# Kernel optimization log

Measured on AMD Instinct MI355X. Metric: run time of the kernel, lower is better.

Reference implementation:

```python
import jax, jax.numpy as jnp
import numpy as np

NUM_BINS = 8
TAIL = 3.0
MBW = 1e-3  # min_bin_width
MBH = 1e-3  # min_bin_height
MD = 1e-3   # min_derivative
B, C, H, W = 16, 12, 128, 128
COND = C // 3
HID = 64
STEP = 3 * NUM_BINS - 1
OUT = C * STEP


def setup_inputs() -> dict:
    key = jax.random.key(0)
    ks = jax.random.split(key, 8)
    s = lambda k, shape, scale=1.0: jax.random.normal(k, shape, jnp.float32) * scale
    return {
        'x': s(ks[0], (B, C, H, W)),
        'logdet': jnp.zeros((B,), jnp.float32),
        'conditioning': s(ks[1], (B, COND, H, W)),
        'W1': s(ks[2], (HID, C + COND, 3, 3), 0.05), 'b1': jnp.zeros((HID,), jnp.float32),
        'W2': s(ks[3], (HID, HID, 1, 1), 0.05), 'b2': jnp.zeros((HID,), jnp.float32),
        'W3': s(ks[4], (OUT, HID, 3, 3), 0.05), 'b3': jnp.zeros((OUT,), jnp.float32),
    }


def _conv(x, w, b, pad):
    y = jax.lax.conv_general_dilated(x, w, (1, 1), [(pad, pad), (pad, pad)],
                                     dimension_numbers=('NCHW', 'OIHW', 'NCHW'))
    return y + b[None, :, None, None]


def _checker_mask(h, w, parity):
    ii, jj = jnp.meshgrid(jnp.arange(h), jnp.arange(w), indexing='ij')
    m = jnp.where((ii + jj) % 2 == 0, parity, 1 - parity)
    return m.astype(jnp.float32)[None, None]  # (1,1,H,W)


def _rqs_forward(x, uw, uh, ud):
    # x: (B,C,H,W); uw/uh: (...,K); ud: (...,K-1). 'linear' tails, tail_bound=TAIL.
    K = NUM_BINS
    left, right = -TAIL, TAIL
    inside = (x >= left) & (x <= right)
    xc = jnp.clip(x, left, right)

    w = MBW + (1.0 - MBW * K) * jax.nn.softmax(uw, axis=-1)
    cw = jnp.pad(jnp.cumsum(w, -1), [(0, 0)] * (w.ndim - 1) + [(1, 0)])
    cw = (right - left) * cw + left
    cw = cw.at[..., 0].set(left).at[..., -1].set(right)
    w = cw[..., 1:] - cw[..., :-1]

    h = MBH + (1.0 - MBH * K) * jax.nn.softmax(uh, axis=-1)
    ch = jnp.pad(jnp.cumsum(h, -1), [(0, 0)] * (h.ndim - 1) + [(1, 0)])
    ch = (right - left) * ch + left
    ch = ch.at[..., 0].set(left).at[..., -1].set(right)
    h = ch[..., 1:] - ch[..., :-1]

    const = float(np.log(np.expm1(1.0 - MD)))  # boundary derivative -> 1 under linear tails
    udp = jnp.pad(ud, [(0, 0)] * (ud.ndim - 1) + [(1, 1)], constant_values=const)
    d = MD + jax.nn.softplus(udp)  # (...,K+1)

    delta = h / w
    # searchsorted: bin index per element
    idx = jnp.clip(jnp.sum((xc[..., None] >= cw).astype(jnp.int32), -1) - 1, 0, K - 1)[..., None]
    g = lambda t: jnp.take_along_axis(t, idx, axis=-1)[..., 0]

    icw, iw = g(cw), g(w)
    ich, ih = g(ch), g(h)
    idl = g(delta)
    id0 = g(d)
    id1 = g(d[..., 1:])

    theta = (xc - icw) / iw
    t1 = theta * (1.0 - theta)
    num = ih * (idl * theta ** 2 + id0 * t1)
    den = idl + (id0 + id1 - 2.0 * idl) * t1
    y = ich + num / den
    dnum = idl ** 2 * (id1 * theta ** 2 + 2.0 * idl * t1 + id0 * (1.0 - theta) ** 2)
    lad = jnp.log(dnum) - 2.0 * jnp.log(den)
    return jnp.where(inside, y, x), jnp.where(inside, lad, 0.0)


def reference(x, logdet, conditioning, W1, b1, W2, b2, W3, b3):
    mask = _checker_mask(H, W, 0)
    x_frozen = mask * x
    x_active = (1.0 - mask) * x
    z = jnp.concatenate([x_frozen, conditioning], axis=1)
    h1 = jax.nn.relu(_conv(z, W1, b1, 1))
    h2 = jax.nn.relu(_conv(h1, W2, b2, 0))
    params = _conv(h2, W3, b3, 1)  # (B, C*STEP, H, W)
    # all channels at once instead of python loop over C
    p = params.reshape(B, C, STEP, H, W).transpose(0, 1, 3, 4, 2)  # (B,C,H,W,STEP)
    uw = p[..., :NUM_BINS]
    uh = p[..., NUM_BINS:2 * NUM_BINS]
    ud = p[..., 2 * NUM_BINS:]
    y, lad = _rqs_forward(x_active, uw, uh, ud)
    x_out = x_frozen + y  # matches original: frozen part + spline output (no re-masking of y)
    logdet_out = logdet + lad.sum(axis=(1, 2, 3))
    return x_out, logdet_out
```

## Files before the change

### kernel.cpp

```cpp
#include <hip/hip_runtime.h>

#define HW (128*128)

typedef __bf16 bf16x8 __attribute__((ext_vector_type(8)));
typedef float  float4v __attribute__((ext_vector_type(4)));
typedef int    int4v   __attribute__((ext_vector_type(4)));
typedef int    int2v   __attribute__((ext_vector_type(2)));

static __device__ __forceinline__ short f2bf(float f) {
    unsigned u = __float_as_uint(f);
    unsigned r = (u + 0x7FFFu + ((u >> 16) & 1u)) >> 16;
    return (short)(r & 0xFFFFu);
}
static __device__ __forceinline__ int pack2(short a, short b) {
    return (int)((unsigned short)a | ((unsigned)(unsigned short)b << 16));
}
static __device__ __forceinline__ void async_cp16(const void* g, void* l) {
    __builtin_amdgcn_global_load_lds(
        (const __attribute__((address_space(1))) unsigned int*)g,
        (__attribute__((address_space(3))) unsigned int*)l, 16, 0, 0);
}

__global__ __launch_bounds__(256) void prep_weights(
    const float* __restrict__ W1, const float* __restrict__ W2,
    const float* __restrict__ W3,
    short* __restrict__ W1sw, short* __restrict__ W2sw, short* __restrict__ W3g,
    char* __restrict__ h2p, int4v* __restrict__ zerobuf)
{
    int tid = blockIdx.x * 256 + threadIdx.x;
    int stride = gridDim.x * 256;
    for (int i = tid; i < 5*256*8; i += stride) {
        int e = i & 7, q = (i >> 3) & 255, s = i >> 11;
        int n = q >> 2, c = q & 3;
        int gc = c ^ ((n >> 1) & 3);
        int tap = 2*s + (gc >> 1);
        int ch = (gc & 1)*8 + e;
        float v = 0.f;
        if (tap < 9) {
            int ky = (tap*11) >> 5; int kx = tap - 3*ky;
            v = W1[((n*16 + ch)*3 + ky)*3 + kx];
        }
        W1sw[i] = f2bf(v);
    }
    for (int i = tid; i < 2*256*8; i += stride) {
        int e = i & 7, q = (i >> 3) & 255, s = i >> 11;
        int n = q >> 2, c = q & 3;
        int gc = c ^ ((n >> 1) & 3);
        int k = s*32 + gc*8 + e;
        W2sw[i] = f2bf(W2[n*64 + k]);
    }
    for (int i = tid; i < 165888; i += stride) {
        int e = i & 7;
        int n = (i >> 3) % 288;
        int r2 = i / 2304;
        int quad = r2 & 3;
        int ks = (r2 >> 2) & 1;
        int tap = r2 >> 3;
        int ch = n / 24, jj = n - 24*ch;
        int kk = ks*32 + quad*8 + e;
        float v = 0.f;
        if (jj < 23) v = W3[((ch*23 + jj)*64 + kk)*9 + tap];
        W3g[i] = f2bf(v);
    }
    for (int i = tid; i < 64; i += stride) { int4v zz = {0,0,0,0}; zerobuf[i] = zz; }
    for (int i = tid; i < 16*516*8; i += stride) {
        int cchunk = i & 7, pxi = (i >> 3) % 516, b = i / (516*8);
        int yy, xx;
        if (pxi < 130)      { yy = 0;   xx = pxi; }
        else if (pxi < 260) { yy = 129; xx = pxi - 130; }
        else if (pxi < 388) { yy = pxi - 260 + 1; xx = 0; }
        else                { yy = pxi - 388 + 1; xx = 129; }
        int4v zz = {0,0,0,0};
        *(int4v*)(h2p + (size_t)((b*130 + yy)*130 + xx)*128 + cchunk*16) = zz;
    }
}

__global__ __launch_bounds__(256) void pack_z(
    const float* __restrict__ x, const float* __restrict__ cond,
    short* __restrict__ zp, float* __restrict__ ldslots)
{
    int id = blockIdx.x * 256 + threadIdx.x;
    if (id < 1024) ldslots[id] = 0.f;
    if (id >= 16*130*130) return;
    int b = id / 16900;
    int rem = id - b*16900;
    int yy = rem / 130;
    int xx = rem - yy*130;
    short vs[16];
    #pragma unroll
    for (int c = 0; c < 16; ++c) vs[c] = 0;
    if (yy >= 1 && yy <= 128 && xx >= 1 && xx <= 128) {
        int pix = (yy - 1)*128 + (xx - 1);
        bool frozen = ((yy + xx) & 1) == 1;
        #pragma unroll
        for (int c = 0; c < 12; ++c)
            vs[c] = f2bf(frozen ? x[(b*12 + c)*HW + pix] : 0.f);
        #pragma unroll
        for (int c = 0; c < 4; ++c)
            vs[12 + c] = f2bf(cond[(b*4 + c)*HW + pix]);
    }
    int4v lo = { pack2(vs[0],vs[1]),  pack2(vs[2],vs[3]),
                 pack2(vs[4],vs[5]),  pack2(vs[6],vs[7]) };
    int4v hi = { pack2(vs[8],vs[9]),  pack2(vs[10],vs[11]),
                 pack2(vs[12],vs[13]),pack2(vs[14],vs[15]) };
    *(int4v*)(zp + id*16)     = lo;
    *(int4v*)(zp + id*16 + 8) = hi;
}

__global__ __launch_bounds__(256, 4) void conv12_kernel(
    const char* __restrict__ zp, const char* __restrict__ W1sw,
    const char* __restrict__ W2sw,
    const float* __restrict__ b1, const float* __restrict__ b2,
    const char* __restrict__ zerobuf, char* __restrict__ h2p)
{
    __shared__ __align__(16) char smem[28672];
    int t = threadIdx.x;
    int lane = t & 63, w = t >> 6;
    int l15 = lane & 15, quad = lane >> 4;
    int bid = blockIdx.x;
    int b = bid & 15, y = bid >> 4;
    int chb = (w >> 1) * 32;
    int pxb = (w & 1) * 64;
    unsigned wbase = (unsigned)__builtin_amdgcn_readfirstlane(w << 10);

    int px1 = t >> 2;
    int gc1 = (t & 3) ^ ((px1 >> 1) & 3);
    int tl1 = gc1 >> 1, zoff1 = px1*32 + (gc1 & 1)*16;
    int q2 = t + 256;
    int px2 = q2 >> 2;
    int gc2 = (q2 & 3) ^ ((px2 >> 1) & 3);
    int tl2 = gc2 >> 1, zoff2 = px2*32 + (gc2 & 1)*16;

    int waddr[2], zaddr[4];
    #pragma unroll
    for (int i = 0; i < 2; ++i) {
        int n = chb + i*16 + l15;
        waddr[i] = 8192 + n*64 + ((quad ^ ((n >> 1) & 3)) << 4);
    }
    #pragma unroll
    for (int j = 0; j < 4; ++j) {
        int px = pxb + j*16 + l15;
        zaddr[j] = px*64 + ((quad ^ ((px >> 1) & 3)) << 4);
    }

    const char* zb = zp + (size_t)(b*16900)*32;
    const float4v z4 = {0.f,0.f,0.f,0.f};
    float4v acc[2][4];
    #pragma unroll
    for (int i = 0; i < 2; ++i)
        #pragma unroll
        for (int j = 0; j < 4; ++j) acc[i][j] = z4;

    for (int s = 0; s < 5; ++s) {
        __syncthreads();
        int ta = 2*s + tl1;
        const char* g1;
        if (ta < 9) { int ky = (ta*11) >> 5; int kx = ta - 3*ky;
            g1 = zb + ((y + ky)*130 + kx)*32 + zoff1; }
        else g1 = zerobuf + (lane << 4);
        async_cp16(g1, smem + wbase);
        int tb = 2*s + tl2;
        const char* g2;
        if (tb < 9) { int ky = (tb*11) >> 5; int kx = tb - 3*ky;
            g2 = zb + ((y + ky)*130 + kx)*32 + zoff2; }
        else g2 = zerobuf + (lane << 4);
        async_cp16(g2, smem + 4096 + wbase);
        async_cp16(W1sw + s*4096 + (t << 4), smem + 8192 + wbase);
        __syncthreads();
        bf16x8 aw[2];
        #pragma unroll
        for (int i = 0; i < 2; ++i) aw[i] = *(const bf16x8*)(smem + waddr[i]);
        #pragma unroll
        for (int j = 0; j < 4; ++j) {
            bf16x8 bzv = *(const bf16x8*)(smem + zaddr[j]);
            #pragma unroll
            for (int i = 0; i < 2; ++i)
                acc[i][j] = __builtin_amdgcn_mfma_f32_16x16x32_bf16(aw[i], bzv, acc[i][j], 0, 0, 0);
        }
    }
    {
        #pragma unroll
        for (int i = 0; i < 2; ++i) {
            int ch0 = chb + i*16 + quad*4;
            float bb0 = b1[ch0], bb1 = b1[ch0+1], bb2 = b1[ch0+2], bb3 = b1[ch0+3];
            #pragma unroll
            for (int j = 0; j < 4; ++j) {
                int px = pxb + j*16 + l15;
                short s0 = f2bf(fmaxf(acc[i][j][0] + bb0, 0.f));
                short s1 = f2bf(fmaxf(acc[i][j][1] + bb1, 0.f));
                short s2 = f2bf(fmaxf(acc[i][j][2] + bb2, 0.f));
                short s3 = f2bf(fmaxf(acc[i][j][3] + bb3, 0.f));
                int2v pk = { pack2(s0, s1), pack2(s2, s3) };
                *(int2v*)(smem + 12288 + px*128 + (((ch0 >> 3) ^ (px & 7)) << 4) + ((ch0 & 7) << 1)) = pk;
            }
        }
    }
    float4v acc2[2][4];
    #pragma unroll
    for (int i = 0; i < 2; ++i)
        #pragma unroll
        for (int j = 0; j < 4; ++j) acc2[i][j] = z4;
    for (int s = 0; s < 2; ++s) {
        __syncthreads();
        async_cp16(W2sw + s*4096 + (t << 4), smem + 8192 + wbase);
        __syncthreads();
        bf16x8 aw[2];
        #pragma unroll
        for (int i = 0; i < 2; ++i) aw[i] = *(const bf16x8*)(smem + waddr[i]);
        #pragma unroll
        for (int j = 0; j < 4; ++j) {
            int px = pxb + j*16 + l15;
            bf16x8 bh = *(const bf16x8*)(smem + 12288 + px*128 + (((s*4 + quad) ^ (px & 7)) << 4));
            #pragma unroll
            for (int i = 0; i < 2; ++i)
                acc2[i][j] = __builtin_amdgcn_mfma_f32_16x16x32_bf16(aw[i], bh, acc2[i][j], 0, 0, 0);
        }
    }
    __syncthreads();
    {
        #pragma unroll
        for (int i = 0; i < 2; ++i) {
            int ch0 = chb + i*16 + quad*4;
            float bb0 = b2[ch0], bb1 = b2[ch0+1], bb2 = b2[ch0+2], bb3 = b2[ch0+3];
            #pragma unroll
            for (int j = 0; j < 4; ++j) {
                int px = pxb + j*16 + l15;
                short s0 = f2bf(fmaxf(acc2[i][j][0] + bb0, 0.f));
                short s1 = f2bf(fmaxf(acc2[i][j][1] + bb1, 0.f));
                short s2 = f2bf(fmaxf(acc2[i][j][2] + bb2, 0.f));
                short s3 = f2bf(fmaxf(acc2[i][j][3] + bb3, 0.f));
                int2v pk = { pack2(s0, s1), pack2(s2, s3) };
                *(int2v*)(smem + 12288 + px*128 + (((ch0 >> 3) ^ (px & 7)) << 4) + ((ch0 & 7) << 1)) = pk;
            }
        }
    }
    __syncthreads();
    char* dst = h2p + ((size_t)(b*130 + y + 1)*130 + 1)*128;
    #pragma unroll
    for (int u = 0; u < 4; ++u) {
        int q = t + u*256;
        int px = q >> 3, g = q & 7;
        int4v v = *(const int4v*)(smem + 12288 + px*128 + ((g ^ (px & 7)) << 4));
        *(int4v*)(dst + px*128 + (g << 4)) = v;
    }
}

static __device__ __forceinline__ float rqs_eval(
    const float* __restrict__ pa, float xin, bool frozen, float& ldsum)
{
    float xa = frozen ? 0.f : xin;
    float xf = frozen ? xin : 0.f;
    float xc = fminf(fmaxf(xa, -3.f), 3.f);
    bool inside = (xa >= -3.f) && (xa <= 3.f);

    float mw = pa[0];
    #pragma unroll
    for (int j = 1; j < 8; ++j) mw = fmaxf(mw, pa[j]);
    float ew[8]; float sw = 0.f;
    #pragma unroll
    for (int j = 0; j < 8; ++j) { ew[j] = __expf(pa[j] - mw); sw += ew[j]; }
    float Aw = 0.992f / sw;
    float run = 0.f, cwl = -3.f, icw = -3.f, iwid = 1.f;
    int idx = 0;
    #pragma unroll
    for (int j = 0; j < 8; ++j) {
        float wj = fmaf(Aw, ew[j], 0.001f);
        run += wj;
        float cwr = (j == 7) ? 3.f : fmaf(6.f, run, -3.f);
        if (xc >= cwl) { icw = cwl; iwid = cwr - cwl; idx = j; }
        cwl = cwr;
    }
    float mh = pa[8];
    #pragma unroll
    for (int j = 9; j < 16; ++j) mh = fmaxf(mh, pa[j]);
    float eh[8]; float sh = 0.f;
    #pragma unroll
    for (int j = 0; j < 8; ++j) { eh[j] = __expf(pa[8 + j] - mh); sh += eh[j]; }
    float Ah = 0.992f / sh;
    run = 0.f;
    float chl = -3.f, ich = 0.f, ihei = 1.f;
    #pragma unroll
    for (int j = 0; j < 8; ++j) {
        float hj = fmaf(Ah, eh[j], 0.001f);
        run += hj;
        float chr = (j == 7) ? 3.f : fmaf(6.f, run, -3.f);
        if (j == idx) { ich = chl; ihei = chr - chl; }
        chl = chr;
    }
    float v0 = 0.f, v1 = 0.f;
    bool h0 = false, h1 = false;
    #pragma unroll
    for (int j = 1; j < 8; ++j) {
        float v = pa[15 + j];
        if (j == idx)     { v0 = v; h0 = true; }
        if (j == idx + 1) { v1 = v; h1 = true; }
    }
    float sp0 = (v0 > 15.f) ? v0 : __logf(1.f + __expf(v0));
    float sp1 = (v1 > 15.f) ? v1 : __logf(1.f + __expf(v1));
    float d0 = h0 ? (0.001f + sp0) : 1.f;
    float d1 = h1 ? (0.001f + sp1) : 1.f;

    float dl = ihei / iwid;
    float th = (xc - icw) / iwid;
    float omt = 1.f - th;
    float t1 = th * omt;
    float num = ihei * (dl*th*th + d0*t1);
    float den = dl + (d0 + d1 - 2.f*dl)*t1;
    float yv = ich + num/den;
    float dnum = dl*dl*(d1*th*th + 2.f*dl*t1 + d0*omt*omt);
    float lad = __logf(dnum) - 2.f*__logf(den);

    ldsum += inside ? lad : 0.f;
    return xf + (inside ? yv : xa);
}

__global__ __launch_bounds__(192, 4) void conv3_rqs_kernel(
    const char* __restrict__ h2p, const char* __restrict__ W3g,
    const float* __restrict__ b3, const float* __restrict__ x,
    float* __restrict__ out, float* __restrict__ ldslots)
{
    __shared__ __align__(16) char smem[27648];
    int t = threadIdx.x;
    int lane = t & 63, w = t >> 6;
    int l15 = lane & 15, quad = lane >> 4;
    int bid = blockIdx.x;
    int b = bid & 15;
    int r = bid >> 4;
    int chalf = r & 1;
    int h = (r >> 1) & 1;
    int y = r >> 2;

    const char* h2pb = h2p + (size_t)(b*130)*130*128;
    int colLo = h*64;
    #pragma unroll
    for (int ii = 0; ii < 9; ++ii) {
        int q = t + ii*192;
        int row = q / 576;
        int rem = q - row*576;
        int p = rem >> 3, cs = rem & 7;
        int cg = cs ^ (p & 7);
        const char* g = h2pb + (((y + row)*130 + colLo + p) << 7) + (cg << 4);
        async_cp16(g, smem + (unsigned)__builtin_amdgcn_readfirstlane(
                                 (w << 10) + ii*3072) + (lane << 4));
    }
    __syncthreads();

    const float4v z4 = {0.f,0.f,0.f,0.f};
    float4v acc[4][3];
    #pragma unroll
    for (int i = 0; i < 4; ++i)
        #pragma unroll
        for (int j = 0; j < 3; ++j) acc[i][j] = z4;

    int bcol = chalf*144 + w*48 + l15;

    for (int tap = 0; tap < 9; ++tap) {
        int ty = (tap*11) >> 5;
        int tx = tap - 3*ty;
        int rowbase = ty*9216;
        #pragma unroll
        for (int ks = 0; ks < 2; ++ks) {
            bf16x8 av[4];
            #pragma unroll
            for (int i = 0; i < 4; ++i) {
                int p = i*16 + l15 + tx;
                av[i] = *(const bf16x8*)(smem + rowbase + (p << 7)
                         + ((((ks << 2) + quad) ^ (p & 7)) << 4));
            }
            const char* bp = W3g
                + ((((tap*2 + ks)*4 + quad)*288 + bcol) << 4);
            #pragma unroll
            for (int j = 0; j < 3; ++j) {
                bf16x8 bv = *(const bf16x8*)(bp + (j << 8));
                #pragma unroll
                for (int i = 0; i < 4; ++i)
                    acc[i][j] = __builtin_amdgcn_mfma_f32_16x16x32_bf16(av[i], bv, acc[i][j], 0, 0, 0);
            }
        }
    }
    __syncthreads();

    float* scr = (float*)smem;
    float ldsum = 0.f;
    int pxl = t & 31;
    int chl = t >> 5;
    int ch = chalf*6 + chl;
    const float* bb3 = b3 + ch*23;

    #pragma unroll
    for (int rnd = 0; rnd < 2; ++rnd) {
        #pragma unroll
        for (int i2 = 0; i2 < 2; ++i2) {
            int i = rnd*2 + i2;
            #pragma unroll
            for (int j = 0; j < 3; ++j)
                #pragma unroll
                for (int rr = 0; rr < 4; ++rr)
                    scr[(i2*16 + quad*4 + rr)*148 + w*48 + j*16 + l15] = acc[i][j][rr];
        }
        __syncthreads();
        const float* P = scr + pxl*148 + chl*24;
        float pa[23];
        {
            float pr[24];
            *(float4v*)&pr[0]  = *(const float4v*)(P);
            *(float4v*)&pr[4]  = *(const float4v*)(P + 4);
            *(float4v*)&pr[8]  = *(const float4v*)(P + 8);
            *(float4v*)&pr[12] = *(const float4v*)(P + 12);
            *(float4v*)&pr[16] = *(const float4v*)(P + 16);
            *(float4v*)&pr[20] = *(const float4v*)(P + 20);
            #pragma unroll
            for (int j = 0; j < 23; ++j) pa[j] = pr[j] + bb3[j];
        }
        int pxg = h*64 + rnd*32 + pxl;
        int gidx = ((b*12 + ch) << 14) + (y << 7) + pxg;
        float xin = x[gidx];
        bool frozen = ((y + pxg) & 1) == 1;
        out[gidx] = rqs_eval(pa, xin, frozen, ldsum);
        __syncthreads();
    }
    #pragma unroll
    for (int off = 32; off > 0; off >>= 1)
        ldsum += __shfl_down(ldsum, off, 64);
    if (lane == 0) atomicAdd(ldslots + b*64 + (r & 63), ldsum);
}

__global__ __launch_bounds__(64) void logdet_reduce(
    const float* __restrict__ ldslots, const float* __restrict__ ld_in,
    float* __restrict__ ldout)
{
    int b = blockIdx.x;
    int lane = threadIdx.x;
    float s = ldslots[b*64 + lane];
    #pragma unroll
    for (int off = 32; off > 0; off >>= 1)
        s += __shfl_down(s, off, 64);
    if (lane == 0) ldout[b] = ld_in[b] + s;
}

extern "C" void kernel_launch(void* const* d_in, const int* in_sizes, int n_in,
                              void* d_out, int out_size, void* d_ws, size_t ws_size,
                              hipStream_t stream)
{
    (void)in_sizes; (void)n_in; (void)out_size; (void)ws_size;
    const float* x    = (const float*)d_in[0];
    const float* ld   = (const float*)d_in[1];
    const float* cond = (const float*)d_in[2];
    const float* W1   = (const float*)d_in[3];
    const float* b1   = (const float*)d_in[4];
    const float* W2   = (const float*)d_in[5];
    const float* b2   = (const float*)d_in[6];
    const float* W3   = (const float*)d_in[7];
    const float* b3   = (const float*)d_in[8];
    float* out = (float*)d_out;
    char* ws = (char*)d_ws;

    short* zp     = (short*)(ws);
    char*  h2p    = ws + 8652800;
    short* W1sw   = (short*)(ws + 43264000);
    short* W2sw   = (short*)(ws + 43284480);
    short* W3g    = (short*)(ws + 43292672);
    char*  zerob  = ws + 43624448;
    float* ldslots= (float*)(ws + 43625472);
    float* ldout  = out + 12*HW*16;

    prep_weights<<<dim3(256), dim3(256), 0, stream>>>(
        W1, W2, W3, W1sw, W2sw, W3g, h2p, (int4v*)zerob);
    pack_z<<<dim3(1057), dim3(256), 0, stream>>>(x, cond, zp, ldslots);
    conv12_kernel<<<dim3(2048), dim3(256), 0, stream>>>(
        (const char*)zp, (const char*)W1sw, (const char*)W2sw, b1, b2,
        (const char*)zerob, h2p);
    conv3_rqs_kernel<<<dim3(8192), dim3(192), 0, stream>>>(
        (const char*)h2p, (const char*)W3g, b3, x, out, ldslots);
    logdet_reduce<<<dim3(16), dim3(64), 0, stream>>>(ldslots, ld, ldout);
}
```

Baseline: 199.8 us.

## Restructure conv1/conv2 kernel: stage input rows once, per-wave tiles, direct weight loads

The conv1+conv2 kernel now loads the three padded input rows into shared memory once per block and forms the 3x3 taps by offset addressing. It no longer re-copies im2col slices per K-step, and the zero buffer is gone. Each wave now owns 32 pixels across all 64 channels. Weights are read straight from global memory in MFMA fragment layout, and each wave keeps its own h1/h2 tile in LDS, which removes most block-wide barriers. The trade-offs are more global weight traffic per wave (served from cache), more accumulator registers, and clamped tap indices for the padded K-step, which depend on the zeroed W1 entries.

```diff
diff --git a/kernel.cpp b/kernel.cpp
--- a/kernel.cpp
+++ b/kernel.cpp
@@ -5,7 +5,6 @@
 typedef __bf16 bf16x8 __attribute__((ext_vector_type(8)));
 typedef float  float4v __attribute__((ext_vector_type(4)));
 typedef int    int4v   __attribute__((ext_vector_type(4)));
-typedef int    int2v   __attribute__((ext_vector_type(2)));
 
 static __device__ __forceinline__ short f2bf(float f) {
     unsigned u = __float_as_uint(f);
@@ -24,30 +23,28 @@
 __global__ __launch_bounds__(256) void prep_weights(
     const float* __restrict__ W1, const float* __restrict__ W2,
     const float* __restrict__ W3,
-    short* __restrict__ W1sw, short* __restrict__ W2sw, short* __restrict__ W3g,
-    char* __restrict__ h2p, int4v* __restrict__ zerobuf)
+    short* __restrict__ W1g, short* __restrict__ W2g, short* __restrict__ W3g,
+    char* __restrict__ h2p)
 {
     int tid = blockIdx.x * 256 + threadIdx.x;
     int stride = gridDim.x * 256;
-    for (int i = tid; i < 5*256*8; i += stride) {
-        int e = i & 7, q = (i >> 3) & 255, s = i >> 11;
-        int n = q >> 2, c = q & 3;
-        int gc = c ^ ((n >> 1) & 3);
-        int tap = 2*s + (gc >> 1);
-        int ch = (gc & 1)*8 + e;
+    for (int i = tid; i < 10240; i += stride) {
+        int e = i & 7, ch = (i >> 3) & 63, sq = i >> 9;
+        int s = sq >> 2, quad = sq & 3;
+        int k = s*32 + quad*8 + e;
+        int tap = k >> 4, ci = k & 15;
         float v = 0.f;
         if (tap < 9) {
             int ky = (tap*11) >> 5; int kx = tap - 3*ky;
-            v = W1[((n*16 + ch)*3 + ky)*3 + kx];
-        }
-        W1sw[i] = f2bf(v);
-    }
-    for (int i = tid; i < 2*256*8; i += stride) {
-        int e = i & 7, q = (i >> 3) & 255, s = i >> 11;
-        int n = q >> 2, c = q & 3;
-        int gc = c ^ ((n >> 1) & 3);
-        int k = s*32 + gc*8 + e;
-        W2sw[i] = f2bf(W2[n*64 + k]);
+            v = W1[((ch*16 + ci)*3 + ky)*3 + kx];
+        }
+        W1g[i] = f2bf(v);
+    }
+    for (int i = tid; i < 4096; i += stride) {
+        int e = i & 7, ch = (i >> 3) & 63, sq = i >> 9;
+        int s = sq >> 2, quad = sq & 3;
+        int k = s*32 + quad*8 + e;
+        W2g[i] = f2bf(W2[ch*64 + k]);
     }
     for (int i = tid; i < 165888; i += stride) {
         int e = i & 7;
@@ -62,7 +59,6 @@
         if (jj < 23) v = W3[((ch*23 + jj)*64 + kk)*9 + tap];
         W3g[i] = f2bf(v);
     }
-    for (int i = tid; i < 64; i += stride) { int4v zz = {0,0,0,0}; zerobuf[i] = zz; }
     for (int i = tid; i < 16*516*8; i += stride) {
         int cchunk = i & 7, pxi = (i >> 3) % 516, b = i / (516*8);
         int yy, xx;
@@ -108,140 +104,121 @@
 }
 
 __global__ __launch_bounds__(256, 4) void conv12_kernel(
-    const char* __restrict__ zp, const char* __restrict__ W1sw,
-    const char* __restrict__ W2sw,
+    const char* __restrict__ zp, const char* __restrict__ W1g,
+    const char* __restrict__ W2g,
     const float* __restrict__ b1, const float* __restrict__ b2,
-    const char* __restrict__ zerobuf, char* __restrict__ h2p)
-{
-    __shared__ __align__(16) char smem[28672];
+    char* __restrict__ h2p)
+{
+    __shared__ __align__(16) char smem[28928];
     int t = threadIdx.x;
     int lane = t & 63, w = t >> 6;
     int l15 = lane & 15, quad = lane >> 4;
     int bid = blockIdx.x;
     int b = bid & 15, y = bid >> 4;
-    int chb = (w >> 1) * 32;
-    int pxb = (w & 1) * 64;
-    unsigned wbase = (unsigned)__builtin_amdgcn_readfirstlane(w << 10);
-
-    int px1 = t >> 2;
-    int gc1 = (t & 3) ^ ((px1 >> 1) & 3);
-    int tl1 = gc1 >> 1, zoff1 = px1*32 + (gc1 & 1)*16;
-    int q2 = t + 256;
-    int px2 = q2 >> 2;
-    int gc2 = (q2 & 3) ^ ((px2 >> 1) & 3);
-    int tl2 = gc2 >> 1, zoff2 = px2*32 + (gc2 & 1)*16;
-
-    int waddr[2], zaddr[4];
-    #pragma unroll
-    for (int i = 0; i < 2; ++i) {
-        int n = chb + i*16 + l15;
-        waddr[i] = 8192 + n*64 + ((quad ^ ((n >> 1) & 3)) << 4);
-    }
-    #pragma unroll
-    for (int j = 0; j < 4; ++j) {
-        int px = pxb + j*16 + l15;
-        zaddr[j] = px*64 + ((quad ^ ((px >> 1) & 3)) << 4);
-    }
-
-    const char* zb = zp + (size_t)(b*16900)*32;
+    int pxb = w << 5;
+
+    const char* zb = (const char*)zp + ((size_t)(b*16900) + (size_t)y*130)*32;
+    #pragma unroll
+    for (int ii = 0; ii < 4; ++ii) {
+        int q = t + ii*256;
+        if (q < 780)
+            async_cp16(zb + (q << 4),
+                smem + (unsigned)__builtin_amdgcn_readfirstlane(
+                            ((w << 6) + ii*256) << 4) + (lane << 4));
+    }
+    __syncthreads();
+
     const float4v z4 = {0.f,0.f,0.f,0.f};
-    float4v acc[2][4];
-    #pragma unroll
-    for (int i = 0; i < 2; ++i)
-        #pragma unroll
-        for (int j = 0; j < 4; ++j) acc[i][j] = z4;
+    char* ht = smem + 12544 + (w << 12);
+
+    float4v acc1[4][2];
+    #pragma unroll
+    for (int i = 0; i < 4; ++i)
+        #pragma unroll
+        for (int j = 0; j < 2; ++j) acc1[i][j] = z4;
 
     for (int s = 0; s < 5; ++s) {
-        __syncthreads();
-        int ta = 2*s + tl1;
-        const char* g1;
-        if (ta < 9) { int ky = (ta*11) >> 5; int kx = ta - 3*ky;
-            g1 = zb + ((y + ky)*130 + kx)*32 + zoff1; }
-        else g1 = zerobuf + (lane << 4);
-        async_cp16(g1, smem + wbase);
-        int tb = 2*s + tl2;
-        const char* g2;
-        if (tb < 9) { int ky = (tb*11) >> 5; int kx = tb - 3*ky;
-            g2 = zb + ((y + ky)*130 + kx)*32 + zoff2; }
-        else g2 = zerobuf + (lane << 4);
-        async_cp16(g2, smem + 4096 + wbase);
-        async_cp16(W1sw + s*4096 + (t << 4), smem + 8192 + wbase);
-        __syncthreads();
-        bf16x8 aw[2];
-        #pragma unroll
-        for (int i = 0; i < 2; ++i) aw[i] = *(const bf16x8*)(smem + waddr[i]);
-        #pragma unroll
-        for (int j = 0; j < 4; ++j) {
-            bf16x8 bzv = *(const bf16x8*)(smem + zaddr[j]);
-            #pragma unroll
-            for (int i = 0; i < 2; ++i)
-                acc[i][j] = __builtin_amdgcn_mfma_f32_16x16x32_bf16(aw[i], bzv, acc[i][j], 0, 0, 0);
+        const char* ap = W1g + (((s*4 + quad)*64 + l15) << 4);
+        bf16x8 aw[4];
+        #pragma unroll
+        for (int i = 0; i < 4; ++i)
+            aw[i] = *(const bf16x8*)(ap + (i << 8));
+        int tap = 2*s + (quad >> 1);
+        int tapc = tap > 8 ? 8 : tap;
+        int ty = (tapc*11) >> 5;
+        int tx = tapc - 3*ty;
+        #pragma unroll
+        for (int j = 0; j < 2; ++j) {
+            int px = pxb + j*16 + l15 + tx;
+            bf16x8 bz = *(const bf16x8*)(smem + ty*4160 + (px << 5) + ((quad & 1) << 4));
+            #pragma unroll
+            for (int i = 0; i < 4; ++i)
+                acc1[i][j] = __builtin_amdgcn_mfma_f32_16x16x32_bf16(aw[i], bz, acc1[i][j], 0, 0, 0);
         }
     }
     {
         #pragma unroll
-        for (int i = 0; i < 2; ++i) {
-            int ch0 = chb + i*16 + quad*4;
-            float bb0 = b1[ch0], bb1 = b1[ch0+1], bb2 = b1[ch0+2], bb3 = b1[ch0+3];
-            #pragma unroll
-            for (int j = 0; j < 4; ++j) {
-                int px = pxb + j*16 + l15;
-                short s0 = f2bf(fmaxf(acc[i][j][0] + bb0, 0.f));
-                short s1 = f2bf(fmaxf(acc[i][j][1] + bb1, 0.f));
-                short s2 = f2bf(fmaxf(acc[i][j][2] + bb2, 0.f));
-                short s3 = f2bf(fmaxf(acc[i][j][3] + bb3, 0.f));
-                int2v pk = { pack2(s0, s1), pack2(s2, s3) };
-                *(int2v*)(smem + 12288 + px*128 + (((ch0 >> 3) ^ (px & 7)) << 4) + ((ch0 & 7) << 1)) = pk;
+        for (int i = 0; i < 4; ++i) {
+            float4v bv = *(const float4v*)(b1 + i*16 + quad*4);
+            int cc = 2*i + (quad >> 1);
+            int wo = ((quad & 1) << 3);
+            #pragma unroll
+            for (int j = 0; j < 2; ++j) {
+                int px = j*16 + l15;
+                int base = (px << 7) + ((cc ^ (px & 7)) << 4) + wo;
+                *(int*)(ht + base)     = pack2(f2bf(fmaxf(acc1[i][j][0] + bv[0], 0.f)),
+                                               f2bf(fmaxf(acc1[i][j][1] + bv[1], 0.f)));
+                *(int*)(ht + base + 4) = pack2(f2bf(fmaxf(acc1[i][j][2] + bv[2], 0.f)),
+                                               f2bf(fmaxf(acc1[i][j][3] + bv[3], 0.f)));
             }
         }
     }
-    float4v acc2[2][4];
-    #pragma unroll
-    for (int i = 0; i < 2; ++i)
-        #pragma unroll
-        for (int j = 0; j < 4; ++j) acc2[i][j] = z4;
+    float4v acc2[4][2];
+    #pragma unroll
+    for (int i = 0; i < 4; ++i)
+        #pragma unroll
+        for (int j = 0; j < 2; ++j) acc2[i][j] = z4;
+
+    #pragma unroll
     for (int s = 0; s < 2; ++s) {
-        __syncthreads();
-        async_cp16(W2sw + s*4096 + (t << 4), smem + 8192 + wbase);
-        __syncthreads();
-        bf16x8 aw[2];
-        #pragma unroll
-        for (int i = 0; i < 2; ++i) aw[i] = *(const bf16x8*)(smem + waddr[i]);
-        #pragma unroll
-        for (int j = 0; j < 4; ++j) {
-            int px = pxb + j*16 + l15;
-            bf16x8 bh = *(const bf16x8*)(smem + 12288 + px*128 + (((s*4 + quad) ^ (px & 7)) << 4));
-            #pragma unroll
-            for (int i = 0; i < 2; ++i)
+        const char* ap = W2g + (((s*4 + quad)*64 + l15) << 4);
+        bf16x8 aw[4];
+        #pragma unroll
+        for (int i = 0; i < 4; ++i)
+            aw[i] = *(const bf16x8*)(ap + (i << 8));
+        #pragma unroll
+        for (int j = 0; j < 2; ++j) {
+            int px = j*16 + l15;
+            bf16x8 bh = *(const bf16x8*)(ht + (px << 7) + (((s*4 + quad) ^ (px & 7)) << 4));
+            #pragma unroll
+            for (int i = 0; i < 4; ++i)
                 acc2[i][j] = __builtin_amdgcn_mfma_f32_16x16x32_bf16(aw[i], bh, acc2[i][j], 0, 0, 0);
         }
     }
-    __syncthreads();
     {
         #pragma unroll
-        for (int i = 0; i < 2; ++i) {
-            int ch0 = chb + i*16 + quad*4;
-            float bb0 = b2[ch0], bb1 = b2[ch0+1], bb2 = b2[ch0+2], bb3 = b2[ch0+3];
-            #pragma unroll
-            for (int j = 0; j < 4; ++j) {
-                int px = pxb + j*16 + l15;
-                short s0 = f2bf(fmaxf(acc2[i][j][0] + bb0, 0.f));
-                short s1 = f2bf(fmaxf(acc2[i][j][1] + bb1, 0.f));
-                short s2 = f2bf(fmaxf(acc2[i][j][2] + bb2, 0.f));
-                short s3 = f2bf(fmaxf(acc2[i][j][3] + bb3, 0.f));
-                int2v pk = { pack2(s0, s1), pack2(s2, s3) };
-                *(int2v*)(smem + 12288 + px*128 + (((ch0 >> 3) ^ (px & 7)) << 4) + ((ch0 & 7) << 1)) = pk;
+        for (int i = 0; i < 4; ++i) {
+            float4v bv = *(const float4v*)(b2 + i*16 + quad*4);
+            int cc = 2*i + (quad >> 1);
+            int wo = ((quad & 1) << 3);
+            #pragma unroll
+            for (int j = 0; j < 2; ++j) {
+                int px = j*16 + l15;
+                int base = (px << 7) + ((cc ^ (px & 7)) << 4) + wo;
+                *(int*)(ht + base)     = pack2(f2bf(fmaxf(acc2[i][j][0] + bv[0], 0.f)),
+                                               f2bf(fmaxf(acc2[i][j][1] + bv[1], 0.f)));
+                *(int*)(ht + base + 4) = pack2(f2bf(fmaxf(acc2[i][j][2] + bv[2], 0.f)),
+                                               f2bf(fmaxf(acc2[i][j][3] + bv[3], 0.f)));
             }
         }
     }
-    __syncthreads();
-    char* dst = h2p + ((size_t)(b*130 + y + 1)*130 + 1)*128;
+    char* dst = h2p + ((size_t)(b*130 + y + 1)*130 + 1 + pxb)*128;
     #pragma unroll
     for (int u = 0; u < 4; ++u) {
-        int q = t + u*256;
-        int px = q >> 3, g = q & 7;
-        int4v v = *(const int4v*)(smem + 12288 + px*128 + ((g ^ (px & 7)) << 4));
-        *(int4v*)(dst + px*128 + (g << 4)) = v;
+        int q = (u << 6) + lane;
+        int px = q >> 3, cc = q & 7;
+        int4v v = *(const int4v*)(ht + (px << 7) + ((cc ^ (px & 7)) << 4));
+        *(int4v*)(dst + (px << 7) + (cc << 4)) = v;
     }
 }
 
@@ -457,19 +434,17 @@
 
     short* zp     = (short*)(ws);
     char*  h2p    = ws + 8652800;
-    short* W1sw   = (short*)(ws + 43264000);
-    short* W2sw   = (short*)(ws + 43284480);
+    short* W1g    = (short*)(ws + 43264000);
+    short* W2g    = (short*)(ws + 43284480);
     short* W3g    = (short*)(ws + 43292672);
-    char*  zerob  = ws + 43624448;
     float* ldslots= (float*)(ws + 43625472);
     float* ldout  = out + 12*HW*16;
 
     prep_weights<<<dim3(256), dim3(256), 0, stream>>>(
-        W1, W2, W3, W1sw, W2sw, W3g, h2p, (int4v*)zerob);
+        W1, W2, W3, W1g, W2g, W3g, h2p);
     pack_z<<<dim3(1057), dim3(256), 0, stream>>>(x, cond, zp, ldslots);
     conv12_kernel<<<dim3(2048), dim3(256), 0, stream>>>(
-        (const char*)zp, (const char*)W1sw, (const char*)W2sw, b1, b2,
-        (const char*)zerob, h2p);
+        (const char*)zp, (const char*)W1g, (const char*)W2g, b1, b2, h2p);
     conv3_rqs_kernel<<<dim3(8192), dim3(192), 0, stream>>>(
         (const char*)h2p, (const char*)W3g, b3, x, out, ldslots);
     logdet_reduce<<<dim3(16), dim3(64), 0, stream>>>(ldslots, ld, ldout);
```

Measured after the change: 202.6 us. No clear change (+1.4%).
